# Performance work log

Hardware: AMD Instinct MI355X
Metric: run time of the kernel (lower is better)

## Reference

```python
import jax, jax.numpy as jnp
import numpy as np

B, D, C = 8192, 2048, 1000
EPS32 = float(np.finfo(np.float32).eps)      # torch clamp_probs uses finfo.eps
LOG_2PI = float(np.log(2.0 * np.pi))
GAMMA = float(1.0 / np.exp(100.0))           # lerp at global_step=0 -> start_val = 1/exp(start_rho)


def setup_inputs() -> dict:
    key = jax.random.key(0)
    k = jax.random.split(key, 6)
    feature = jax.random.normal(k[0], (B, D), jnp.float32)
    target = jax.random.randint(k[1], (B,), 0, C)
    eps = jax.random.normal(k[2], (B, D), jnp.float32)
    # y_project: Linear(C, D) -> weight [D, C], bias [D]
    y_w = jax.random.normal(k[3], (D, C), jnp.float32) * 0.02
    y_b = jnp.zeros((D,), jnp.float32)
    # cls_project: Linear(D, C) -> weight [C, D], bias [C]
    # small weights + positive bias keep Categorical probs positive (torch would
    # clamp negatives to eps; we replicate the clamp but avoid degenerate NaNs)
    cls_w = jax.random.normal(k[4], (C, D), jnp.float32) * 0.001
    cls_b = jnp.ones((C,), jnp.float32) * 5.0
    return dict(feature=feature, y_w=y_w, y_b=y_b, cls_w=cls_w, cls_b=cls_b,
                eps=eps, target=target)


def reference(feature, y_w, y_b, cls_w, cls_b, eps, target):
    # z = m.sample() : identity-covariance MVN sample, detached (torch .sample())
    z = jax.lax.stop_gradient(feature + eps)                      # [B, D]

    # y_emb = y_project(one_hot(target)) == gather of weight columns + bias
    y_emb = jnp.take(y_w, target, axis=1).T + y_b                 # [B, D]

    # Categorical(probs=cls_project(z)): normalize, clamp, log
    probs_raw = z @ cls_w.T + cls_b                               # [B, C]
    p = probs_raw / jnp.sum(probs_raw, axis=-1, keepdims=True)
    logits = jnp.log(jnp.clip(p, EPS32, 1.0 - EPS32))             # [B, C]

    # identity-covariance MVN log_prob in closed form
    const = 0.5 * D * LOG_2PI
    h1 = 0.5 * jnp.sum((z - feature) ** 2, axis=-1) + const       # -m.log_prob(z)
    h2 = 0.5 * jnp.sum((z - y_emb) ** 2, axis=-1) + const         # -y_emb_d.log_prob(z)
    h3 = -jnp.take_along_axis(logits, target[:, None], axis=1)[:, 0]

    rex = h2 - h1
    loss = jnp.mean(jnp.float32(GAMMA) * rex + h3)
    return logits, loss
```

## Files before the change

### kernel.cpp

```cpp
#include <hip/hip_runtime.h>
#include <hip/hip_bf16.h>

#define B_ROWS 8192
#define D_DIM  2048
#define C_DIM  1000
#define C_PAD  1024

#define EPS32   1.1920928955078125e-07f

typedef __attribute__((ext_vector_type(8))) short short8;
typedef __attribute__((ext_vector_type(4))) float f32x4;

#define GLOAD_LDS16(gptr, lptr) \
  __builtin_amdgcn_global_load_lds((const __attribute__((address_space(1))) void*)(gptr), \
                                   (__attribute__((address_space(3))) void*)(lptr), 16, 0, 0)

__device__ inline unsigned short f2bf(float x) {
  union { __hip_bfloat16 b; unsigned short u; } cv;
  cv.b = __float2bfloat16(x);
  return cv.u;
}

__device__ inline float wave_red(float v) {
#pragma unroll
  for (int off = 32; off > 0; off >>= 1) v += __shfl_down(v, off, 64);
  return v;
}

#define ZBLK 8192
__global__ __launch_bounds__(256) void fuse_z(const float4* __restrict__ f4,
                                              const float4* __restrict__ e4,
                                              uint4* __restrict__ z4,
                                              const float* __restrict__ cls_w,
                                              __hip_bfloat16* __restrict__ clsw_bf) {
  int bid = blockIdx.x;
  if (bid < ZBLK) {
    int t = bid * 256 + threadIdx.x;
    int i0 = t * 2;
    float4 f0 = f4[i0], f1 = f4[i0 + 1];
    float4 e0 = e4[i0], e1 = e4[i0 + 1];
    union { unsigned short u[8]; uint4 v; } pz;
    pz.u[0] = f2bf(f0.x + e0.x);
    pz.u[1] = f2bf(f0.y + e0.y);
    pz.u[2] = f2bf(f0.z + e0.z);
    pz.u[3] = f2bf(f0.w + e0.w);
    pz.u[4] = f2bf(f1.x + e1.x);
    pz.u[5] = f2bf(f1.y + e1.y);
    pz.u[6] = f2bf(f1.z + e1.z);
    pz.u[7] = f2bf(f1.w + e1.w);
    z4[t] = pz.v;
  } else {
    int j = ((bid - ZBLK) * 256 + threadIdx.x) * 8;
    int row = j >> 11;
    int col = j & 2047;
    union { unsigned short u[8]; uint4 v; } pk;
    if (row < C_DIM) {
      const float* src = cls_w + (size_t)row * D_DIM + col;
#pragma unroll
      for (int i2 = 0; i2 < 8; ++i2) pk.u[i2] = f2bf(src[i2]);
    } else {
#pragma unroll
      for (int i2 = 0; i2 < 8; ++i2) pk.u[i2] = 0;
    }
    *(uint4*)((unsigned short*)clsw_bf + j) = pk.v;
  }
}

__global__ __launch_bounds__(256) void gemm_bt(const __hip_bfloat16* __restrict__ A,
                                               const __hip_bfloat16* __restrict__ Bt,
                                               const float* __restrict__ cls_b,
                                               float* __restrict__ out) {
  __shared__ __align__(16) __hip_bfloat16 sA[128 * 64];
  __shared__ __align__(16) __hip_bfloat16 sB[64 * 64];
  const int tid = threadIdx.x;
  const int m0 = blockIdx.x * 128;
  const int n0 = blockIdx.y * 64;
  const int w = tid >> 6, lane = tid & 63;
  const int wm = (w & 1) * 64, wn = (w >> 1) * 32;
  const int l15 = lane & 15, quad = lane >> 4;

  f32x4 acc[4][2] = {};

  for (int k0 = 0; k0 < D_DIM; k0 += 64) {
#pragma unroll
    for (int i = 0; i < 4; ++i) {
      int j = i * 256 + tid;
      int row = j >> 3;
      int cc = (j & 7) ^ (row & 7);
      GLOAD_LDS16(A + (size_t)(m0 + row) * D_DIM + k0 + cc * 8, &sA[j * 8]);
    }
#pragma unroll
    for (int i = 0; i < 2; ++i) {
      int j = i * 256 + tid;
      int row = j >> 3;
      int cc = (j & 7) ^ (row & 7);
      GLOAD_LDS16(Bt + (size_t)(n0 + row) * D_DIM + k0 + cc * 8, &sB[j * 8]);
    }
    __syncthreads();
#pragma unroll
    for (int kk = 0; kk < 64; kk += 32) {
      const int ccr = (kk >> 3) + quad;
      short8 af[4], bfr[2];
#pragma unroll
      for (int i = 0; i < 4; ++i) {
        int r = wm + i * 16 + l15;
        af[i] = *(const short8*)&sA[(r * 8 + (ccr ^ (r & 7))) * 8];
      }
#pragma unroll
      for (int jn = 0; jn < 2; ++jn) {
        int r = wn + jn * 16 + l15;
        bfr[jn] = *(const short8*)&sB[(r * 8 + (ccr ^ (r & 7))) * 8];
      }
#pragma unroll
      for (int i = 0; i < 4; ++i)
#pragma unroll
        for (int jn = 0; jn < 2; ++jn)
          acc[i][jn] = __builtin_amdgcn_mfma_f32_16x16x32_bf16(af[i], bfr[jn], acc[i][jn], 0, 0, 0);
    }
    __syncthreads();
  }

#pragma unroll
  for (int i = 0; i < 4; ++i) {
    int row = m0 + wm + i * 16 + quad * 4;
#pragma unroll
    for (int jn = 0; jn < 2; ++jn) {
      int col = n0 + wn + jn * 16 + l15;
      if (col < C_DIM) {
        float bias = cls_b[col];
#pragma unroll
        for (int r = 0; r < 4; ++r)
          out[(size_t)(row + r) * C_DIM + col] = acc[i][jn][r] + bias;
      }
    }
  }
}

__global__ __launch_bounds__(256) void rownorm(float* __restrict__ out,
                                               const int* __restrict__ target,
                                               float* __restrict__ rowloss) {
  const int wv = threadIdx.x >> 6, lane = threadIdx.x & 63;
  const int r0 = blockIdx.x * 16 + wv * 4;

  float v[4][16];
#pragma unroll
  for (int rr = 0; rr < 4; ++rr) {
    const float* row = out + (size_t)(r0 + rr) * C_DIM;
#pragma unroll
    for (int k = 0; k < 4; ++k) {
      int c = k * 256 + lane * 4;
      if (c + 3 < C_DIM) {
        float4 f = *(const float4*)(row + c);
        v[rr][k * 4 + 0] = f.x; v[rr][k * 4 + 1] = f.y;
        v[rr][k * 4 + 2] = f.z; v[rr][k * 4 + 3] = f.w;
      } else {
#pragma unroll
        for (int i = 0; i < 4; ++i) v[rr][k * 4 + i] = (c + i < C_DIM) ? row[c + i] : 0.f;
      }
    }
  }

  float s[4];
#pragma unroll
  for (int rr = 0; rr < 4; ++rr) {
    float a = 0.f;
#pragma unroll
    for (int k = 0; k < 16; ++k) a += v[rr][k];
    s[rr] = a;
  }
#pragma unroll
  for (int rr = 0; rr < 4; ++rr) {
#pragma unroll
    for (int off = 32; off > 0; off >>= 1) s[rr] += __shfl_down(s[rr], off, 64);
    s[rr] = __shfl(s[rr], 0, 64);
  }

  int tg[4];
#pragma unroll
  for (int rr = 0; rr < 4; ++rr) tg[rr] = target[r0 + rr];

#pragma unroll
  for (int rr = 0; rr < 4; ++rr) {
    float inv = 1.0f / s[rr];
    float* row = out + (size_t)(r0 + rr) * C_DIM;
#pragma unroll
    for (int k = 0; k < 4; ++k) {
      int c = k * 256 + lane * 4;
      float lg[4];
#pragma unroll
      for (int i = 0; i < 4; ++i) {
        float p = v[rr][k * 4 + i] * inv;
        p = fminf(fmaxf(p, EPS32), 1.0f - EPS32);
        lg[i] = __logf(p);
        if (c + i == tg[rr]) rowloss[r0 + rr] = -lg[i];
      }
      if (c + 3 < C_DIM) {
        *(float4*)(row + c) = make_float4(lg[0], lg[1], lg[2], lg[3]);
      } else {
#pragma unroll
        for (int i = 0; i < 4; ++i) if (c + i < C_DIM) row[c + i] = lg[i];
      }
    }
  }
}

__global__ __launch_bounds__(1024) void finalize(const float* __restrict__ rowloss,
                                                 float* __restrict__ out_loss) {
  int tid = threadIdx.x;
  float a[8];
#pragma unroll
  for (int j = 0; j < 8; ++j) a[j] = rowloss[tid + j * 1024];
  float s = 0.f;
#pragma unroll
  for (int j = 0; j < 8; ++j) s += a[j];
  s = wave_red(s);
  __shared__ float sm[16];
  if ((tid & 63) == 0) sm[tid >> 6] = s;
  __syncthreads();
  if (tid == 0) {
    float t = 0.f;
#pragma unroll
    for (int k = 0; k < 16; ++k) t += sm[k];
    out_loss[0] = t * (1.0f / B_ROWS);
  }
}

extern "C" void kernel_launch(void* const* d_in, const int* in_sizes, int n_in,
                              void* d_out, int out_size, void* d_ws, size_t ws_size,
                              hipStream_t stream) {
  const float* feature = (const float*)d_in[0];
  const float* cls_w   = (const float*)d_in[3];
  const float* cls_b   = (const float*)d_in[4];
  const float* eps     = (const float*)d_in[5];
  const int*   target  = (const int*)d_in[6];
  float* out = (float*)d_out;
  float* out_loss = out + (size_t)B_ROWS * C_DIM;

  char* ws = (char*)d_ws;
  __hip_bfloat16* z_bf    = (__hip_bfloat16*)ws;
  __hip_bfloat16* clsw_bf = (__hip_bfloat16*)(ws + 33554432);
  float*          rowloss = (float*)(ws + 33554432 + 4194304);

  fuse_z<<<dim3(ZBLK + 1024), 256, 0, stream>>>((const float4*)feature, (const float4*)eps,
                                                (uint4*)z_bf, cls_w, clsw_bf);
  gemm_bt<<<dim3(B_ROWS / 128, C_PAD / 64), 256, 0, stream>>>(z_bf, clsw_bf, cls_b, out);
  rownorm<<<dim3(B_ROWS / 16), 256, 0, stream>>>(out, target, rowloss);
  finalize<<<dim3(1), 1024, 0, stream>>>(rowloss, out_loss);
}
```

Before: 232.8 us.

## Double-buffer LDS tiles in bf16 GEMM to overlap loads with MFMA

The GEMM kernel now uses two LDS buffers for A and B tiles and issues the global-to-LDS loads for the next K step before computing on the current one, leaving one barrier per iteration. Global addresses are precomputed once outside the loop, and launch bounds now request 3 blocks per CU. The aim is to hide global load latency behind MFMA work. Doubling LDS to 48KB per block may limit occupancy. Because __syncthreads may not wait on the async LDS loads, correctness rests on the barrier's implicit vmcnt wait.

```diff
diff --git a/kernel.cpp b/kernel.cpp
--- a/kernel.cpp
+++ b/kernel.cpp
@@ -66,12 +66,12 @@
   }
 }
 
-__global__ __launch_bounds__(256) void gemm_bt(const __hip_bfloat16* __restrict__ A,
-                                               const __hip_bfloat16* __restrict__ Bt,
-                                               const float* __restrict__ cls_b,
-                                               float* __restrict__ out) {
-  __shared__ __align__(16) __hip_bfloat16 sA[128 * 64];
-  __shared__ __align__(16) __hip_bfloat16 sB[64 * 64];
+__global__ __launch_bounds__(256, 3) void gemm_bt(const __hip_bfloat16* __restrict__ A,
+                                                  const __hip_bfloat16* __restrict__ Bt,
+                                                  const float* __restrict__ cls_b,
+                                                  float* __restrict__ out) {
+  __shared__ __align__(16) __hip_bfloat16 sA[2][128 * 64];
+  __shared__ __align__(16) __hip_bfloat16 sB[2][64 * 64];
   const int tid = threadIdx.x;
   const int m0 = blockIdx.x * 128;
   const int n0 = blockIdx.y * 64;
@@ -79,24 +79,34 @@
   const int wm = (w & 1) * 64, wn = (w >> 1) * 32;
   const int l15 = lane & 15, quad = lane >> 4;
 
+  const __hip_bfloat16* As[4]; int ja[4];
+  const __hip_bfloat16* Bs[2]; int jb[2];
+#pragma unroll
+  for (int i = 0; i < 4; ++i) {
+    int j = i * 256 + tid;
+    int row = j >> 3;
+    int cc = (j & 7) ^ (row & 7);
+    As[i] = A + (size_t)(m0 + row) * D_DIM + cc * 8;
+    ja[i] = j * 8;
+  }
+#pragma unroll
+  for (int i = 0; i < 2; ++i) {
+    int j = i * 256 + tid;
+    int row = j >> 3;
+    int cc = (j & 7) ^ (row & 7);
+    Bs[i] = Bt + (size_t)(n0 + row) * D_DIM + cc * 8;
+    jb[i] = j * 8;
+  }
+
   f32x4 acc[4][2] = {};
 
-  for (int k0 = 0; k0 < D_DIM; k0 += 64) {
-#pragma unroll
-    for (int i = 0; i < 4; ++i) {
-      int j = i * 256 + tid;
-      int row = j >> 3;
-      int cc = (j & 7) ^ (row & 7);
-      GLOAD_LDS16(A + (size_t)(m0 + row) * D_DIM + k0 + cc * 8, &sA[j * 8]);
-    }
-#pragma unroll
-    for (int i = 0; i < 2; ++i) {
-      int j = i * 256 + tid;
-      int row = j >> 3;
-      int cc = (j & 7) ^ (row & 7);
-      GLOAD_LDS16(Bt + (size_t)(n0 + row) * D_DIM + k0 + cc * 8, &sB[j * 8]);
-    }
-    __syncthreads();
+  auto STAGE = [&](int buf, int k0) {
+#pragma unroll
+    for (int i = 0; i < 4; ++i) GLOAD_LDS16(As[i] + k0, &sA[buf][ja[i]]);
+#pragma unroll
+    for (int i = 0; i < 2; ++i) GLOAD_LDS16(Bs[i] + k0, &sB[buf][jb[i]]);
+  };
+  auto COMPUTE = [&](const __hip_bfloat16* cA, const __hip_bfloat16* cB) {
 #pragma unroll
     for (int kk = 0; kk < 64; kk += 32) {
       const int ccr = (kk >> 3) + quad;
@@ -104,12 +114,12 @@
 #pragma unroll
       for (int i = 0; i < 4; ++i) {
         int r = wm + i * 16 + l15;
-        af[i] = *(const short8*)&sA[(r * 8 + (ccr ^ (r & 7))) * 8];
+        af[i] = *(const short8*)&cA[(r * 8 + (ccr ^ (r & 7))) * 8];
       }
 #pragma unroll
       for (int jn = 0; jn < 2; ++jn) {
         int r = wn + jn * 16 + l15;
-        bfr[jn] = *(const short8*)&sB[(r * 8 + (ccr ^ (r & 7))) * 8];
+        bfr[jn] = *(const short8*)&cB[(r * 8 + (ccr ^ (r & 7))) * 8];
       }
 #pragma unroll
       for (int i = 0; i < 4; ++i)
@@ -117,7 +127,16 @@
         for (int jn = 0; jn < 2; ++jn)
           acc[i][jn] = __builtin_amdgcn_mfma_f32_16x16x32_bf16(af[i], bfr[jn], acc[i][jn], 0, 0, 0);
     }
+  };
+
+  STAGE(0, 0);
+  __syncthreads();
+  int cur = 0;
+  for (int k0 = 0; k0 < D_DIM; k0 += 64) {
+    if (k0 + 64 < D_DIM) STAGE(cur ^ 1, k0 + 64);
+    COMPUTE(sA[cur], sB[cur]);
     __syncthreads();
+    cur ^= 1;
   }
 
 #pragma unroll
```

New measurement: 247.3 us. +6.2%, slower.

## Precompute row sums via z·colsum(W) and fuse log-normalization into GEMM epilogue

Applied to the files above, without the earlier changes.

The row sum of z@W^T+b is computed algebraically as z·sum_c(W[c]) + sum(b) inside the z conversion kernel, using a new prep kernel that reduces the cls_w columns. This lets the GEMM epilogue normalize, clamp, take the log and record the target loss directly, which removes the separate rownorm pass that re-read and re-wrote the 32 MB logits tensor. The cost is an extra column-sum pass over cls_w, a per-row dot product, and scattered scalar stores in the epilogue. The row sum now comes from a different summation order than the GEMM, which could cause small numerical differences.

```diff
diff --git a/kernel.cpp b/kernel.cpp
--- a/kernel.cpp
+++ b/kernel.cpp
@@ -21,36 +21,26 @@
   return cv.u;
 }
 
+__device__ inline float bf2f(unsigned short u) {
+  union { unsigned int i; float f; } c;
+  c.i = (unsigned int)u << 16;
+  return c.f;
+}
+
 __device__ inline float wave_red(float v) {
 #pragma unroll
   for (int off = 32; off > 0; off >>= 1) v += __shfl_down(v, off, 64);
   return v;
 }
 
-#define ZBLK 8192
-__global__ __launch_bounds__(256) void fuse_z(const float4* __restrict__ f4,
-                                              const float4* __restrict__ e4,
-                                              uint4* __restrict__ z4,
-                                              const float* __restrict__ cls_w,
-                                              __hip_bfloat16* __restrict__ clsw_bf) {
-  int bid = blockIdx.x;
-  if (bid < ZBLK) {
-    int t = bid * 256 + threadIdx.x;
-    int i0 = t * 2;
-    float4 f0 = f4[i0], f1 = f4[i0 + 1];
-    float4 e0 = e4[i0], e1 = e4[i0 + 1];
-    union { unsigned short u[8]; uint4 v; } pz;
-    pz.u[0] = f2bf(f0.x + e0.x);
-    pz.u[1] = f2bf(f0.y + e0.y);
-    pz.u[2] = f2bf(f0.z + e0.z);
-    pz.u[3] = f2bf(f0.w + e0.w);
-    pz.u[4] = f2bf(f1.x + e1.x);
-    pz.u[5] = f2bf(f1.y + e1.y);
-    pz.u[6] = f2bf(f1.z + e1.z);
-    pz.u[7] = f2bf(f1.w + e1.w);
-    z4[t] = pz.v;
-  } else {
-    int j = ((bid - ZBLK) * 256 + threadIdx.x) * 8;
+__global__ __launch_bounds__(256) void prep(const float* __restrict__ cls_w,
+                                            __hip_bfloat16* __restrict__ clsw_bf,
+                                            const float* __restrict__ cls_b,
+                                            float* __restrict__ wsum,
+                                            float* __restrict__ bsum) {
+  int bid = blockIdx.x, tid = threadIdx.x;
+  if (bid < 1024) {
+    int j = (bid * 256 + tid) * 8;
     int row = j >> 11;
     int col = j & 2047;
     union { unsigned short u[8]; uint4 v; } pk;
@@ -63,13 +53,78 @@
       for (int i2 = 0; i2 < 8; ++i2) pk.u[i2] = 0;
     }
     *(uint4*)((unsigned short*)clsw_bf + j) = pk.v;
-  }
+  } else if (bid < 1088) {
+    int k = bid - 1024;
+    int col = k * 32 + (tid & 31);
+    int g = tid >> 5;
+    float s = 0.f;
+    const float* p = cls_w + (size_t)(g * 125) * D_DIM + col;
+#pragma unroll 5
+    for (int rr = 0; rr < 125; ++rr) s += p[(size_t)rr * D_DIM];
+    __shared__ float lsm[8][32];
+    lsm[g][tid & 31] = s;
+    __syncthreads();
+    if (tid < 32) {
+      float a = 0.f;
+#pragma unroll
+      for (int gg = 0; gg < 8; ++gg) a += lsm[gg][tid];
+      wsum[k * 32 + tid] = a;
+    }
+  } else {
+    float s = 0.f;
+    int i0 = tid * 4;
+    if (i0 < C_DIM)
+      s = cls_b[i0] + cls_b[i0 + 1] + cls_b[i0 + 2] + cls_b[i0 + 3];
+    s = wave_red(s);
+    __shared__ float sm[4];
+    if ((tid & 63) == 0) sm[tid >> 6] = s;
+    __syncthreads();
+    if (tid == 0) bsum[0] = sm[0] + sm[1] + sm[2] + sm[3];
+  }
+}
+
+__global__ __launch_bounds__(256) void fuse_z(const float4* __restrict__ f4,
+                                              const float4* __restrict__ e4,
+                                              uint4* __restrict__ z4,
+                                              const float* __restrict__ wsum,
+                                              const float* __restrict__ bsum,
+                                              float* __restrict__ rowsum) {
+  int bid = blockIdx.x, tid = threadIdx.x;
+  int t = bid * 256 + tid;
+  int i0 = t * 2;
+  float4 f0 = f4[i0], f1 = f4[i0 + 1];
+  float4 e0 = e4[i0], e1 = e4[i0 + 1];
+  float4 w0 = *(const float4*)(wsum + tid * 8);
+  float4 w1 = *(const float4*)(wsum + tid * 8 + 4);
+  union { unsigned short u[8]; uint4 v; } pz;
+  pz.u[0] = f2bf(f0.x + e0.x);
+  pz.u[1] = f2bf(f0.y + e0.y);
+  pz.u[2] = f2bf(f0.z + e0.z);
+  pz.u[3] = f2bf(f0.w + e0.w);
+  pz.u[4] = f2bf(f1.x + e1.x);
+  pz.u[5] = f2bf(f1.y + e1.y);
+  pz.u[6] = f2bf(f1.z + e1.z);
+  pz.u[7] = f2bf(f1.w + e1.w);
+  z4[t] = pz.v;
+
+  float d = bf2f(pz.u[0]) * w0.x + bf2f(pz.u[1]) * w0.y +
+            bf2f(pz.u[2]) * w0.z + bf2f(pz.u[3]) * w0.w +
+            bf2f(pz.u[4]) * w1.x + bf2f(pz.u[5]) * w1.y +
+            bf2f(pz.u[6]) * w1.z + bf2f(pz.u[7]) * w1.w;
+  d = wave_red(d);
+  __shared__ float sm[4];
+  if ((tid & 63) == 0) sm[tid >> 6] = d;
+  __syncthreads();
+  if (tid == 0) rowsum[bid] = sm[0] + sm[1] + sm[2] + sm[3] + bsum[0];
 }
 
 __global__ __launch_bounds__(256) void gemm_bt(const __hip_bfloat16* __restrict__ A,
                                                const __hip_bfloat16* __restrict__ Bt,
                                                const float* __restrict__ cls_b,
-                                               float* __restrict__ out) {
+                                               const float* __restrict__ rowsum,
+                                               const int* __restrict__ target,
+                                               float* __restrict__ out,
+                                               float* __restrict__ rowloss) {
   __shared__ __align__(16) __hip_bfloat16 sA[128 * 64];
   __shared__ __align__(16) __hip_bfloat16 sB[64 * 64];
   const int tid = threadIdx.x;
@@ -120,85 +175,30 @@
     __syncthreads();
   }
 
+  float bias[2]; int bcol[2];
+#pragma unroll
+  for (int jn = 0; jn < 2; ++jn) {
+    bcol[jn] = n0 + wn + jn * 16 + l15;
+    bias[jn] = (bcol[jn] < C_DIM) ? cls_b[bcol[jn]] : 0.f;
+  }
 #pragma unroll
   for (int i = 0; i < 4; ++i) {
-    int row = m0 + wm + i * 16 + quad * 4;
-#pragma unroll
-    for (int jn = 0; jn < 2; ++jn) {
-      int col = n0 + wn + jn * 16 + l15;
-      if (col < C_DIM) {
-        float bias = cls_b[col];
-#pragma unroll
-        for (int r = 0; r < 4; ++r)
-          out[(size_t)(row + r) * C_DIM + col] = acc[i][jn][r] + bias;
-      }
-    }
-  }
-}
-
-__global__ __launch_bounds__(256) void rownorm(float* __restrict__ out,
-                                               const int* __restrict__ target,
-                                               float* __restrict__ rowloss) {
-  const int wv = threadIdx.x >> 6, lane = threadIdx.x & 63;
-  const int r0 = blockIdx.x * 16 + wv * 4;
-
-  float v[4][16];
-#pragma unroll
-  for (int rr = 0; rr < 4; ++rr) {
-    const float* row = out + (size_t)(r0 + rr) * C_DIM;
-#pragma unroll
-    for (int k = 0; k < 4; ++k) {
-      int c = k * 256 + lane * 4;
-      if (c + 3 < C_DIM) {
-        float4 f = *(const float4*)(row + c);
-        v[rr][k * 4 + 0] = f.x; v[rr][k * 4 + 1] = f.y;
-        v[rr][k * 4 + 2] = f.z; v[rr][k * 4 + 3] = f.w;
-      } else {
-#pragma unroll
-        for (int i = 0; i < 4; ++i) v[rr][k * 4 + i] = (c + i < C_DIM) ? row[c + i] : 0.f;
-      }
-    }
-  }
-
-  float s[4];
-#pragma unroll
-  for (int rr = 0; rr < 4; ++rr) {
-    float a = 0.f;
-#pragma unroll
-    for (int k = 0; k < 16; ++k) a += v[rr][k];
-    s[rr] = a;
-  }
-#pragma unroll
-  for (int rr = 0; rr < 4; ++rr) {
-#pragma unroll
-    for (int off = 32; off > 0; off >>= 1) s[rr] += __shfl_down(s[rr], off, 64);
-    s[rr] = __shfl(s[rr], 0, 64);
-  }
-
-  int tg[4];
-#pragma unroll
-  for (int rr = 0; rr < 4; ++rr) tg[rr] = target[r0 + rr];
-
-#pragma unroll
-  for (int rr = 0; rr < 4; ++rr) {
-    float inv = 1.0f / s[rr];
-    float* row = out + (size_t)(r0 + rr) * C_DIM;
-#pragma unroll
-    for (int k = 0; k < 4; ++k) {
-      int c = k * 256 + lane * 4;
-      float lg[4];
-#pragma unroll
-      for (int i = 0; i < 4; ++i) {
-        float p = v[rr][k * 4 + i] * inv;
-        p = fminf(fmaxf(p, EPS32), 1.0f - EPS32);
-        lg[i] = __logf(p);
-        if (c + i == tg[rr]) rowloss[r0 + rr] = -lg[i];
-      }
-      if (c + 3 < C_DIM) {
-        *(float4*)(row + c) = make_float4(lg[0], lg[1], lg[2], lg[3]);
-      } else {
-#pragma unroll
-        for (int i = 0; i < 4; ++i) if (c + i < C_DIM) row[c + i] = lg[i];
+#pragma unroll
+    for (int r = 0; r < 4; ++r) {
+      int row = m0 + wm + i * 16 + quad * 4 + r;
+      float inv = 1.0f / rowsum[row];
+      int tg = target[row];
+      float* orow = out + (size_t)row * C_DIM;
+#pragma unroll
+      for (int jn = 0; jn < 2; ++jn) {
+        int col = bcol[jn];
+        if (col < C_DIM) {
+          float p = (acc[i][jn][r] + bias[jn]) * inv;
+          p = fminf(fmaxf(p, EPS32), 1.0f - EPS32);
+          float lg = __logf(p);
+          orow[col] = lg;
+          if (col == tg) rowloss[row] = -lg;
+        }
       }
     }
   }
@@ -239,11 +239,15 @@
   char* ws = (char*)d_ws;
   __hip_bfloat16* z_bf    = (__hip_bfloat16*)ws;
   __hip_bfloat16* clsw_bf = (__hip_bfloat16*)(ws + 33554432);
-  float*          rowloss = (float*)(ws + 33554432 + 4194304);
-
-  fuse_z<<<dim3(ZBLK + 1024), 256, 0, stream>>>((const float4*)feature, (const float4*)eps,
-                                                (uint4*)z_bf, cls_w, clsw_bf);
-  gemm_bt<<<dim3(B_ROWS / 128, C_PAD / 64), 256, 0, stream>>>(z_bf, clsw_bf, cls_b, out);
-  rownorm<<<dim3(B_ROWS / 16), 256, 0, stream>>>(out, target, rowloss);
+  float*          rowloss = (float*)(ws + 37748736);
+  float*          rowsum  = (float*)(ws + 37781504);
+  float*          wsum    = (float*)(ws + 37814272);
+  float*          bsum    = (float*)(ws + 37822464);
+
+  prep<<<dim3(1024 + 64 + 1), 256, 0, stream>>>(cls_w, clsw_bf, cls_b, wsum, bsum);
+  fuse_z<<<dim3(B_ROWS), 256, 0, stream>>>((const float4*)feature, (const float4*)eps,
+                                           (uint4*)z_bf, wsum, bsum, rowsum);
+  gemm_bt<<<dim3(B_ROWS / 128, C_PAD / 64), 256, 0, stream>>>(z_bf, clsw_bf, cls_b,
+                                                              rowsum, target, out, rowloss);
   finalize<<<dim3(1), 1024, 0, stream>>>(rowloss, out_loss);
 }
```

Result: slower. 240.5 us (+3.3%).
